# Optimization experiments

Measured on AMD Instinct MI355X. Metric: run time of the kernel, lower is better.

## Reference

```python
import jax, jax.numpy as jnp
import numpy as np

N = 100000      # nodes
E = 1600000     # edges (avg degree 16)
F_IN = 64       # num_features
HID = 16        # hidden channels (fixed in module)
OUT = 32        # num_classes
K = 2           # kernel_size (dim=1, degree=1 open B-spline -> 2 basis fns)


def setup_inputs() -> dict:
    key = jax.random.key(0)
    ks = jax.random.split(key, 8)
    return {
        "x": jax.random.normal(ks[0], (N, F_IN), jnp.float32),
        "edge_index": jax.random.randint(ks[1], (2, E), 0, N, dtype=jnp.int64),
        "dropout": 0,  # unused in eval mode (F.dropout training=False)
        "edge_attr": jnp.full((E, 1), 0.1, jnp.float32),  # nt([0.1]) broadcast per edge
        "W1": jax.random.normal(ks[2], (K, F_IN, HID), jnp.float32) / np.sqrt(K * F_IN).astype(np.float32),
        "root1": jax.random.normal(ks[3], (F_IN, HID), jnp.float32) / np.sqrt(F_IN).astype(np.float32),
        "bias1": jnp.zeros((HID,), jnp.float32),
        "W2": jax.random.normal(ks[4], (K, HID, OUT), jnp.float32) / np.sqrt(K * HID).astype(np.float32),
        "root2": jax.random.normal(ks[5], (HID, OUT), jnp.float32) / np.sqrt(HID).astype(np.float32),
        "bias2": jnp.zeros((OUT,), jnp.float32),
    }


def spline_conv(x, edge_index, edge_attr, W, root, bias):
    """SplineConv, dim=1, kernel_size=2, degree=1 open B-spline, aggr='mean'."""
    src, dst = edge_index[0], edge_index[1]
    n = x.shape[0]
    u = edge_attr[:, 0]                                  # [E] pseudo-coords in [0,1]
    # degree-1 open spline, kernel_size=2: frac = u*(ks-1) = u; kernels {0,1}
    basis = jnp.stack([1.0 - u, u], axis=1)              # [E, K]
    # transform at node level (cheaper than gathering raw features per edge)
    h = jnp.einsum('nf,kfo->nko', x, W)                  # [N, K, out]
    msg = jnp.einsum('ek,eko->eo', basis, h[src])        # [E, out]
    summed = jax.ops.segment_sum(msg, dst, num_segments=n)
    deg = jax.ops.segment_sum(jnp.ones_like(u), dst, num_segments=n)
    out = summed / jnp.maximum(deg, 1.0)[:, None]        # mean aggregation
    return out + x @ root + bias                          # root weight + bias


def reference(x, edge_index, dropout, edge_attr, W1, root1, bias1, W2, root2, bias2):
    # dropout is a no-op in eval mode
    h = jax.nn.elu(spline_conv(x, edge_index, edge_attr, W1, root1, bias1))
    h = spline_conv(h, edge_index, edge_attr, W2, root2, bias2)
    return jax.nn.log_softmax(h, axis=1)
```

## Files before the change

### kernel.cpp

```cpp
#include <hip/hip_runtime.h>
#include <math.h>

#define NN 100000
#define NE 1600000
#define F_IN 64
#define HID 16
#define OUTF 32
#define BKT_SHIFT 6
#define BKT_NODES 64
#define NBKT 1563
#define SRCM 0x1FFFF
#define CAP_REG 2048
#define CAP_LDS 1536
#define PBLK2 500
#define EPB2 3200
#define OVF_MAX 4096

__device__ __forceinline__ unsigned bf16r(float f) {
    unsigned u = __float_as_uint(f);
    return (u + 0x7FFFu + ((u >> 16) & 1u)) >> 16;
}
__device__ __forceinline__ float bfa(unsigned p) { return __uint_as_float(p << 16); }
__device__ __forceinline__ float bfd(unsigned p) { return __uint_as_float(p & 0xFFFF0000u); }
__device__ __forceinline__ float bfh(unsigned short v) { return __uint_as_float(((unsigned)v) << 16); }

__device__ __forceinline__ void acc8(uint4 hv, float u, float* s0, float* s1) {
    unsigned w[4] = {hv.x, hv.y, hv.z, hv.w};
#pragma unroll
    for (int q = 0; q < 4; ++q) {
        float lo = __uint_as_float(w[q] << 16);
        float hi = __uint_as_float(w[q] & 0xFFFF0000u);
        s0[2 * q]     += lo; s1[2 * q]     = fmaf(u, lo, s1[2 * q]);
        s0[2 * q + 1] += hi; s1[2 * q + 1] = fmaf(u, hi, s1[2 * q + 1]);
    }
}
__device__ __forceinline__ void acc4(uint4 ap, float u, float* a) {
    unsigned w[4] = {ap.x, ap.y, ap.z, ap.w};
#pragma unroll
    for (int q = 0; q < 4; ++q)
        a[q] += fmaf(u, bfd(w[q]), bfa(w[q]));
}

__global__ __launch_bounds__(256) void zeroG_kernel(int* __restrict__ gcur,
                                                    int* __restrict__ novf) {
    int t = blockIdx.x * 256 + threadIdx.x;
    if (t < NBKT) gcur[t] = 0;
    if (t == NBKT) novf[0] = 0;
}

__global__ __launch_bounds__(1024) void partF_kernel(const int* __restrict__ ei,
                                                     const float* __restrict__ ea,
                                                     int* __restrict__ gcur,
                                                     int* __restrict__ novf,
                                                     int4* __restrict__ ovf,
                                                     int2* __restrict__ bkt) {
    __shared__ int hcnt[NBKT];
    __shared__ int hbase[NBKT];
    __shared__ int lbase[NBKT];
    __shared__ int s[1024];
    __shared__ int2 sbuf[EPB2];
    __shared__ unsigned short bid[EPB2];
    int t = threadIdx.x, blk = blockIdx.x;
    for (int i = t; i < NBKT; i += 1024) hcnt[i] = 0;
    __syncthreads();
    int beg = blk * EPB2;
    int4 d4 = make_int4(0, 0, 0, 0);
    bool act = (4 * t) < EPB2;
    if (act) {
        d4 = *(const int4*)(ei + NE + beg + 4 * t);
        atomicAdd(&hcnt[d4.x >> BKT_SHIFT], 1);
        atomicAdd(&hcnt[d4.y >> BKT_SHIFT], 1);
        atomicAdd(&hcnt[d4.z >> BKT_SHIFT], 1);
        atomicAdd(&hcnt[d4.w >> BKT_SHIFT], 1);
    }
    __syncthreads();
    int i0 = 2 * t, i1 = 2 * t + 1;
    int v0 = (i0 < NBKT) ? hcnt[i0] : 0;
    int v1 = (i1 < NBKT) ? hcnt[i1] : 0;
    s[t] = v0 + v1;
    __syncthreads();
    for (int off = 1; off < 1024; off <<= 1) {
        int xv = (t >= off) ? s[t - off] : 0;
        __syncthreads();
        s[t] += xv;
        __syncthreads();
    }
    int run = (t == 0) ? 0 : s[t - 1];
    if (i0 < NBKT) lbase[i0] = run;
    if (i1 < NBKT) lbase[i1] = run + v0;
    __syncthreads();
    for (int i = t; i < NBKT; i += 1024) {
        int c = hcnt[i];
        hbase[i] = c ? atomicAdd(&gcur[i], c) : 0;
        hcnt[i] = 0;
    }
    __syncthreads();
    if (act) {
        int4 s4 = *(const int4*)(ei + beg + 4 * t);
        float4 u4 = *(const float4*)(ea + beg + 4 * t);
        int dst[4] = {d4.x, d4.y, d4.z, d4.w};
        int src[4] = {s4.x, s4.y, s4.z, s4.w};
        float uu[4] = {u4.x, u4.y, u4.z, u4.w};
#pragma unroll
        for (int k = 0; k < 4; ++k) {
            int b = dst[k] >> BKT_SHIFT;
            int r = atomicAdd(&hcnt[b], 1);
            int lp = lbase[b] + r;
            sbuf[lp] = make_int2(src[k] | ((dst[k] & (BKT_NODES - 1)) << 17),
                                 __float_as_int(uu[k]));
            bid[lp] = (unsigned short)b;
        }
    }
    __syncthreads();
    for (int i = t; i < EPB2; i += 1024) {
        int2 pk = sbuf[i];
        int b = bid[i];
        int p = hbase[b] + (i - lbase[b]);
        if (p < CAP_REG) {
            bkt[(size_t)b * CAP_REG + p] = pk;
        } else {
            int o = atomicAdd(novf, 1);
            if (o < OVF_MAX)
                ovf[o] = make_int4(b * BKT_NODES + (((unsigned)pk.x) >> 17), pk.x & SRCM, pk.y, 0);
        }
    }
}

__global__ __launch_bounds__(256) void proj1_kernel(const float* __restrict__ x,
                                                    const float* __restrict__ W1,
                                                    const float* __restrict__ root1,
                                                    const float* __restrict__ bias1,
                                                    unsigned* __restrict__ ab1p,
                                                    float* __restrict__ r1) {
    __shared__ float w[2 * F_IN * HID];
    __shared__ float wr[F_IN * HID];
    __shared__ float bb[HID];
    for (int i = threadIdx.x; i < 2 * F_IN * HID; i += 256) w[i] = W1[i];
    for (int i = threadIdx.x; i < F_IN * HID; i += 256) wr[i] = root1[i];
    if (threadIdx.x < HID) bb[threadIdx.x] = bias1[threadIdx.x];
    __syncthreads();
    int n = blockIdx.x * 256 + threadIdx.x;
    if (n >= NN) return;
    float accA[HID], accB[HID], accR[HID];
#pragma unroll
    for (int o = 0; o < HID; ++o) { accA[o] = 0.f; accB[o] = 0.f; accR[o] = bb[o]; }
    const float4* xr4 = (const float4*)(x + (size_t)n * F_IN);
    for (int f4 = 0; f4 < F_IN / 4; ++f4) {
        float4 xv4 = xr4[f4];
        float xs[4] = {xv4.x, xv4.y, xv4.z, xv4.w};
#pragma unroll
        for (int q = 0; q < 4; ++q) {
            int f = f4 * 4 + q;
            float xv = xs[q];
            const float* w0 = &w[f * HID];
            const float* w1 = &w[F_IN * HID + f * HID];
            const float* w2 = &wr[f * HID];
#pragma unroll
            for (int o = 0; o < HID; ++o) {
                accA[o] = fmaf(xv, w0[o], accA[o]);
                accB[o] = fmaf(xv, w1[o], accB[o]);
                accR[o] = fmaf(xv, w2[o], accR[o]);
            }
        }
    }
    unsigned* ar = ab1p + (size_t)n * HID;
    float* rr = r1 + (size_t)n * HID;
#pragma unroll
    for (int o = 0; o < HID; ++o) {
        ar[o] = bf16r(accA[o]) | (bf16r(accB[o] - accA[o]) << 16);
        rr[o] = accR[o];
    }
}

__global__ __launch_bounds__(256) void gather1_kernel(const int* __restrict__ gcur,
                                                      const int* __restrict__ novf,
                                                      const int4* __restrict__ ovf,
                                                      int2* __restrict__ bkt,
                                                      const unsigned* __restrict__ ab1p,
                                                      const float* __restrict__ r1,
                                                      unsigned short* __restrict__ h16,
                                                      float* __restrict__ dinv,
                                                      int* __restrict__ segg) {
    __shared__ int2 sorted[CAP_LDS];
    __shared__ int cnt[BKT_NODES], cur[BKT_NODES], segb[BKT_NODES + 1];
    __shared__ float degsL[BKT_NODES];
    int t = threadIdx.x;
    int b = blockIdx.x;
    int tot = gcur[b];
    int beg = b * CAP_REG;
    if (t < BKT_NODES) { cnt[t] = 0; cur[t] = 0; degsL[t] = 0.f; }
    __syncthreads();
    int nodeBase = b * BKT_NODES;

    if (tot <= CAP_LDS) {
        for (int e = t; e < tot; e += 256)
            atomicAdd(&cnt[((unsigned)bkt[beg + e].x) >> 17], 1);
        __syncthreads();
        if (t < BKT_NODES) {
            int v = cnt[t];
            int sc = v;
#pragma unroll
            for (int off = 1; off < 64; off <<= 1) {
                int o = __shfl_up(sc, off, 64);
                if (t >= off) sc += o;
            }
            segb[t] = sc - v;
            if (t == 63) segb[64] = sc;
        }
        __syncthreads();
        for (int e = t; e < tot; e += 256) {
            int2 pk = bkt[beg + e];
            int loc = ((unsigned)pk.x) >> 17;
            int pos = segb[loc] + atomicAdd(&cur[loc], 1);
            sorted[pos] = pk;
        }
        __syncthreads();
        int nv = tot >> 1;
        int4* s4 = (int4*)sorted;
        int4* o4 = (int4*)(bkt + beg);
        for (int i = t; i < nv; i += 256) o4[i] = s4[i];
        if (t == 0 && (tot & 1)) bkt[beg + tot - 1] = sorted[tot - 1];
        if (t <= BKT_NODES) segg[b * (BKT_NODES + 1) + t] = segb[t];
        int node = t >> 2;
        int jq = t & 3;
        int s0 = segb[node], e2 = segb[node + 1];
        float acc[4] = {0.f, 0.f, 0.f, 0.f};
        int e = s0;
        for (; e + 3 < e2; e += 4) {
            int2 p0 = sorted[e];
            int2 p1 = sorted[e + 1];
            int2 p2 = sorted[e + 2];
            int2 p3 = sorted[e + 3];
            uint4 a0 = *(const uint4*)(ab1p + ((size_t)(p0.x & SRCM) << 4) + (jq << 2));
            uint4 a1 = *(const uint4*)(ab1p + ((size_t)(p1.x & SRCM) << 4) + (jq << 2));
            uint4 a2 = *(const uint4*)(ab1p + ((size_t)(p2.x & SRCM) << 4) + (jq << 2));
            uint4 a3 = *(const uint4*)(ab1p + ((size_t)(p3.x & SRCM) << 4) + (jq << 2));
            acc4(a0, __int_as_float(p0.y), acc);
            acc4(a1, __int_as_float(p1.y), acc);
            acc4(a2, __int_as_float(p2.y), acc);
            acc4(a3, __int_as_float(p3.y), acc);
        }
        for (; e < e2; ++e) {
            int2 pk = sorted[e];
            uint4 ap = *(const uint4*)(ab1p + ((size_t)(pk.x & SRCM) << 4) + (jq << 2));
            acc4(ap, __int_as_float(pk.y), acc);
        }
        int n = nodeBase + node;
        if (n < NN) {
            float d0 = 1.f / (float)max(e2 - s0, 1);
            float4 rv = *(const float4*)(r1 + ((size_t)n << 4) + (jq << 2));
            float rr[4] = {rv.x, rv.y, rv.z, rv.w};
            unsigned hw[4];
#pragma unroll
            for (int k = 0; k < 4; ++k) {
                float v = acc[k] * d0 + rr[k];
                hw[k] = bf16r(v > 0.f ? v : expm1f(v));
            }
            *(uint2*)(h16 + ((size_t)n << 4) + (jq << 2)) =
                make_uint2(hw[0] | (hw[1] << 16), hw[2] | (hw[3] << 16));
            if (jq == 0) dinv[n] = d0;
        }
    } else {
        float* accL = (float*)sorted;
        int inreg = min(tot, CAP_REG);
        int end = beg + inreg;
        for (int i = t; i < BKT_NODES * HID; i += 256) accL[i] = 0.f;
        __syncthreads();
        int j = t & (HID - 1);
        int g = t >> 4;
        for (int e = beg + g; e < end; e += 16) {
            int2 pk = bkt[e];
            unsigned p = ab1p[(size_t)(pk.x & SRCM) * HID + j];
            atomicAdd(&accL[(((unsigned)pk.x) >> 17) * HID + j],
                      fmaf(__int_as_float(pk.y), bfd(p), bfa(p)));
            if (j == 0) atomicAdd(&degsL[((unsigned)pk.x) >> 17], 1.f);
        }
        int ovn = min(novf[0], OVF_MAX);
        for (int o = 0; o < ovn; ++o) {
            int4 ent = ovf[o];
            int loc = ent.x - nodeBase;
            if (loc >= 0 && loc < BKT_NODES && g == 0) {
                unsigned p = ab1p[(size_t)ent.y * HID + j];
                atomicAdd(&accL[loc * HID + j], fmaf(__int_as_float(ent.z), bfd(p), bfa(p)));
                if (j == 0) atomicAdd(&degsL[loc], 1.f);
            }
        }
        __syncthreads();
        if (t < BKT_NODES) degsL[t] = 1.f / fmaxf(degsL[t], 1.f);
        if (t == 0) segg[b * (BKT_NODES + 1)] = -1;
        __syncthreads();
        for (int idx = t; idx < BKT_NODES * HID; idx += 256) {
            int nl = idx >> 4, jj = idx & (HID - 1);
            int n = nodeBase + nl;
            if (n < NN) {
                float v = accL[idx] * degsL[nl] + r1[(size_t)n * HID + jj];
                h16[(size_t)n * HID + jj] = (unsigned short)bf16r(v > 0.f ? v : expm1f(v));
            }
        }
        if (t < BKT_NODES && nodeBase + t < NN) dinv[nodeBase + t] = degsL[t];
    }
}

#define HB_NODES 32
__global__ __launch_bounds__(256) void gather2_kernel(const int* __restrict__ gcur,
                                                      const int* __restrict__ novf,
                                                      const int4* __restrict__ ovf,
                                                      const int2* __restrict__ bkt,
                                                      const unsigned short* __restrict__ h16,
                                                      const float* __restrict__ W2,
                                                      const float* __restrict__ root2,
                                                      const float* __restrict__ bias2,
                                                      const float* __restrict__ dinv,
                                                      const int* __restrict__ segg,
                                                      float* __restrict__ out) {
    __shared__ int segb[HB_NODES + 1];
    __shared__ int sflag;
    __shared__ float s0L[HB_NODES * HID];
    __shared__ float s1L[HB_NODES * HID];
    __shared__ float hloc[HB_NODES * HID];
    __shared__ float w20[HID * OUTF], w2d[HID * OUTF], wr[HID * OUTF];
    __shared__ float bb[OUTF];
    int t = threadIdx.x;
    int b2 = blockIdx.x;
    int b = b2 >> 1;
    int h = b2 & 1;
    for (int i = t; i < HID * OUTF; i += 256) {
        float a = W2[i];
        w20[i] = a;
        w2d[i] = W2[HID * OUTF + i] - a;
        wr[i] = root2[i];
    }
    if (t < OUTF) bb[t] = bias2[t];
    int tot = gcur[b];
    int beg = b * CAP_REG;
    int nodeBase = b * BKT_NODES + h * HB_NODES;
    if (t <= HB_NODES) segb[t] = segg[b * (BKT_NODES + 1) + h * HB_NODES + t];
    if (t == 0) sflag = segg[b * (BKT_NODES + 1)];
    if (t < HB_NODES * HID / 8) {
        uint4 hv = *(const uint4*)(h16 + ((size_t)nodeBase << 4) + t * 8);
        unsigned w4[4] = {hv.x, hv.y, hv.z, hv.w};
#pragma unroll
        for (int q = 0; q < 4; ++q) {
            hloc[t * 8 + 2 * q]     = __uint_as_float(w4[q] << 16);
            hloc[t * 8 + 2 * q + 1] = __uint_as_float(w4[q] & 0xFFFF0000u);
        }
    }
    __syncthreads();

    if (tot <= CAP_LDS && sflag != -1) {
        const int2* sp = bkt + beg;
        int node = t >> 3;
        int sub = (t >> 1) & 3;
        int jh = t & 1;
        int s = segb[node], e2 = segb[node + 1];
        float s0[8] = {0.f, 0.f, 0.f, 0.f, 0.f, 0.f, 0.f, 0.f};
        float s1[8] = {0.f, 0.f, 0.f, 0.f, 0.f, 0.f, 0.f, 0.f};
        int e = s + sub;
        for (; e + 12 < e2; e += 16) {
            int2 p0 = sp[e];
            int2 p1 = sp[e + 4];
            int2 p2 = sp[e + 8];
            int2 p3 = sp[e + 12];
            uint4 h0 = *(const uint4*)(h16 + ((size_t)(p0.x & SRCM) << 4) + (jh << 3));
            uint4 h1 = *(const uint4*)(h16 + ((size_t)(p1.x & SRCM) << 4) + (jh << 3));
            uint4 h2 = *(const uint4*)(h16 + ((size_t)(p2.x & SRCM) << 4) + (jh << 3));
            uint4 h3 = *(const uint4*)(h16 + ((size_t)(p3.x & SRCM) << 4) + (jh << 3));
            acc8(h0, __int_as_float(p0.y), s0, s1);
            acc8(h1, __int_as_float(p1.y), s0, s1);
            acc8(h2, __int_as_float(p2.y), s0, s1);
            acc8(h3, __int_as_float(p3.y), s0, s1);
        }
        for (; e < e2; e += 4) {
            int2 pk = sp[e];
            uint4 hv = *(const uint4*)(h16 + ((size_t)(pk.x & SRCM) << 4) + (jh << 3));
            acc8(hv, __int_as_float(pk.y), s0, s1);
        }
#pragma unroll
        for (int k = 0; k < 8; ++k) {
            s0[k] += __shfl_xor(s0[k], 2); s0[k] += __shfl_xor(s0[k], 4);
            s1[k] += __shfl_xor(s1[k], 2); s1[k] += __shfl_xor(s1[k], 4);
        }
        if (sub == 0) {
            int base = node * HID + jh * 8;
#pragma unroll
            for (int k = 0; k < 8; ++k) { s0L[base + k] = s0[k]; s1L[base + k] = s1[k]; }
        }
        __syncthreads();
    } else {
        int inreg = min(tot, CAP_REG);
        int end = beg + inreg;
        for (int i = t; i < HB_NODES * HID; i += 256) { s0L[i] = 0.f; s1L[i] = 0.f; }
        __syncthreads();
        int j = t & (HID - 1);
        int g = t >> 4;
        for (int e = beg + g; e < end; e += 16) {
            int2 pk = bkt[e];
            int loc = ((unsigned)pk.x) >> 17;
            if ((loc >> 5) == h) {
                float hvv = bfh(h16[(size_t)(pk.x & SRCM) * HID + j]);
                atomicAdd(&s0L[(loc & 31) * HID + j], hvv);
                atomicAdd(&s1L[(loc & 31) * HID + j], __int_as_float(pk.y) * hvv);
            }
        }
        int ovn = min(novf[0], OVF_MAX);
        for (int o = 0; o < ovn; ++o) {
            int4 ent = ovf[o];
            int loc = ent.x - nodeBase;
            if (loc >= 0 && loc < HB_NODES && g == 0) {
                float hvv = bfh(h16[(size_t)ent.y * HID + j]);
                atomicAdd(&s0L[loc * HID + j], hvv);
                atomicAdd(&s1L[loc * HID + j], __int_as_float(ent.z) * hvv);
            }
        }
        __syncthreads();
    }

#pragma unroll
    for (int it = 0; it < HB_NODES * OUTF / 256; ++it) {
        int idx = it * 256 + t;
        int nl = idx >> 5, jj = idx & (OUTF - 1);
        int n = nodeBase + nl;
        float v = 0.f;
        if (n < NN) {
            float msum = 0.f;
            const float* S0 = &s0L[nl * HID];
            const float* S1 = &s1L[nl * HID];
#pragma unroll
            for (int f = 0; f < HID; ++f)
                msum += S0[f] * w20[f * OUTF + jj] + S1[f] * w2d[f * OUTF + jj];
            v = msum * dinv[n] + bb[jj];
            const float* hr = &hloc[nl * HID];
#pragma unroll
            for (int f = 0; f < HID; ++f)
                v = fmaf(hr[f], wr[f * OUTF + jj], v);
        }
        float m = v;
#pragma unroll
        for (int mask = 16; mask >= 1; mask >>= 1) m = fmaxf(m, __shfl_xor(m, mask));
        float ex = expf(v - m);
        float sm = ex;
#pragma unroll
        for (int mask = 16; mask >= 1; mask >>= 1) sm += __shfl_xor(sm, mask);
        if (n < NN) out[(size_t)n * OUTF + jj] = v - m - logf(sm);
    }
}

extern "C" void kernel_launch(void* const* d_in, const int* in_sizes, int n_in,
                              void* d_out, int out_size, void* d_ws, size_t ws_size,
                              hipStream_t stream) {
    const float* x     = (const float*)d_in[0];
    const int*   ei    = (const int*)d_in[1];
    const float* ea    = (const float*)d_in[3];
    const float* W1    = (const float*)d_in[4];
    const float* root1 = (const float*)d_in[5];
    const float* bias1 = (const float*)d_in[6];
    const float* W2    = (const float*)d_in[7];
    const float* root2 = (const float*)d_in[8];
    const float* bias2 = (const float*)d_in[9];
    float* out = (float*)d_out;
    float* ws  = (float*)d_ws;

    const size_t N = NN;
    int*            gcur = (int*)(ws);
    int*            novf = (int*)(ws + 2000);
    int4*           ovf  = (int4*)(ws + 2048);
    float*          dinv = ws + 20000;
    int*            segg = (int*)(ws + 120000);
    float*          r1   = ws + 222000;
    unsigned*       ab1p = (unsigned*)(ws + 222000 + 16 * N);
    unsigned short* h16  = (unsigned short*)(ws + 222000 + 32 * N);
    int2*           bkt  = (int2*)(ws + 222000 + 40 * N);

    int nbN = (NN + 255) / 256;
    zeroG_kernel<<<(NBKT + 256) / 256, 256, 0, stream>>>(gcur, novf);
    partF_kernel<<<PBLK2, 1024, 0, stream>>>(ei, ea, gcur, novf, ovf, bkt);
    proj1_kernel<<<nbN, 256, 0, stream>>>(x, W1, root1, bias1, ab1p, r1);
    gather1_kernel<<<NBKT, 256, 0, stream>>>(gcur, novf, ovf, bkt, ab1p, r1, h16, dinv, segg);
    gather2_kernel<<<NBKT * 2, 256, 0, stream>>>(gcur, novf, ovf, bkt, h16, W2, root2, bias2, dinv, segg, out);
}
```

Measured before the change: 120.0 us.

## Keep gathered sums in registers and compute epilogue per node-thread group

```diff
diff --git a/kernel.cpp b/kernel.cpp
--- a/kernel.cpp
+++ b/kernel.cpp
@@ -11,7 +11,7 @@
 #define NBKT 1563
 #define SRCM 0x1FFFF
 #define CAP_REG 2048
-#define CAP_LDS 1536
+#define CAP_LDS 1184
 #define PBLK2 500
 #define EPB2 3200
 #define OVF_MAX 4096
@@ -313,13 +313,10 @@
                                                       const float* __restrict__ dinv,
                                                       const int* __restrict__ segg,
                                                       float* __restrict__ out) {
+    __shared__ float w20[HID * OUTF], w2d[HID * OUTF], wr[HID * OUTF];
+    __shared__ float bb[OUTF];
     __shared__ int segb[HB_NODES + 1];
     __shared__ int sflag;
-    __shared__ float s0L[HB_NODES * HID];
-    __shared__ float s1L[HB_NODES * HID];
-    __shared__ float hloc[HB_NODES * HID];
-    __shared__ float w20[HID * OUTF], w2d[HID * OUTF], wr[HID * OUTF];
-    __shared__ float bb[OUTF];
     int t = threadIdx.x;
     int b2 = blockIdx.x;
     int b = b2 >> 1;
@@ -336,25 +333,18 @@
     int nodeBase = b * BKT_NODES + h * HB_NODES;
     if (t <= HB_NODES) segb[t] = segg[b * (BKT_NODES + 1) + h * HB_NODES + t];
     if (t == 0) sflag = segg[b * (BKT_NODES + 1)];
-    if (t < HB_NODES * HID / 8) {
-        uint4 hv = *(const uint4*)(h16 + ((size_t)nodeBase << 4) + t * 8);
-        unsigned w4[4] = {hv.x, hv.y, hv.z, hv.w};
-#pragma unroll
-        for (int q = 0; q < 4; ++q) {
-            hloc[t * 8 + 2 * q]     = __uint_as_float(w4[q] << 16);
-            hloc[t * 8 + 2 * q + 1] = __uint_as_float(w4[q] & 0xFFFF0000u);
-        }
-    }
-    __syncthreads();
+    __syncthreads();
+
+    int node = t >> 3;
+    int li = t & 7;
+    int sub = li >> 1;
+    int jh = li & 1;
+    float S0[8] = {0.f, 0.f, 0.f, 0.f, 0.f, 0.f, 0.f, 0.f};
+    float S1[8] = {0.f, 0.f, 0.f, 0.f, 0.f, 0.f, 0.f, 0.f};
 
     if (tot <= CAP_LDS && sflag != -1) {
         const int2* sp = bkt + beg;
-        int node = t >> 3;
-        int sub = (t >> 1) & 3;
-        int jh = t & 1;
         int s = segb[node], e2 = segb[node + 1];
-        float s0[8] = {0.f, 0.f, 0.f, 0.f, 0.f, 0.f, 0.f, 0.f};
-        float s1[8] = {0.f, 0.f, 0.f, 0.f, 0.f, 0.f, 0.f, 0.f};
         int e = s + sub;
         for (; e + 12 < e2; e += 16) {
             int2 p0 = sp[e];
@@ -365,34 +355,30 @@
             uint4 h1 = *(const uint4*)(h16 + ((size_t)(p1.x & SRCM) << 4) + (jh << 3));
             uint4 h2 = *(const uint4*)(h16 + ((size_t)(p2.x & SRCM) << 4) + (jh << 3));
             uint4 h3 = *(const uint4*)(h16 + ((size_t)(p3.x & SRCM) << 4) + (jh << 3));
-            acc8(h0, __int_as_float(p0.y), s0, s1);
-            acc8(h1, __int_as_float(p1.y), s0, s1);
-            acc8(h2, __int_as_float(p2.y), s0, s1);
-            acc8(h3, __int_as_float(p3.y), s0, s1);
+            acc8(h0, __int_as_float(p0.y), S0, S1);
+            acc8(h1, __int_as_float(p1.y), S0, S1);
+            acc8(h2, __int_as_float(p2.y), S0, S1);
+            acc8(h3, __int_as_float(p3.y), S0, S1);
         }
         for (; e < e2; e += 4) {
             int2 pk = sp[e];
             uint4 hv = *(const uint4*)(h16 + ((size_t)(pk.x & SRCM) << 4) + (jh << 3));
-            acc8(hv, __int_as_float(pk.y), s0, s1);
+            acc8(hv, __int_as_float(pk.y), S0, S1);
         }
 #pragma unroll
         for (int k = 0; k < 8; ++k) {
-            s0[k] += __shfl_xor(s0[k], 2); s0[k] += __shfl_xor(s0[k], 4);
-            s1[k] += __shfl_xor(s1[k], 2); s1[k] += __shfl_xor(s1[k], 4);
-        }
-        if (sub == 0) {
-            int base = node * HID + jh * 8;
-#pragma unroll
-            for (int k = 0; k < 8; ++k) { s0L[base + k] = s0[k]; s1L[base + k] = s1[k]; }
-        }
-        __syncthreads();
+            S0[k] += __shfl_xor(S0[k], 2); S0[k] += __shfl_xor(S0[k], 4);
+            S1[k] += __shfl_xor(S1[k], 2); S1[k] += __shfl_xor(S1[k], 4);
+        }
     } else {
+        float* s0L = w20;
+        float* s1L = w2d;
+        for (int i = t; i < HB_NODES * HID; i += 256) { s0L[i] = 0.f; s1L[i] = 0.f; }
+        __syncthreads();
+        int j = t & (HID - 1);
+        int g = t >> 4;
         int inreg = min(tot, CAP_REG);
         int end = beg + inreg;
-        for (int i = t; i < HB_NODES * HID; i += 256) { s0L[i] = 0.f; s1L[i] = 0.f; }
-        __syncthreads();
-        int j = t & (HID - 1);
-        int g = t >> 4;
         for (int e = beg + g; e < end; e += 16) {
             int2 pk = bkt[e];
             int loc = ((unsigned)pk.x) >> 17;
@@ -413,35 +399,70 @@
             }
         }
         __syncthreads();
-    }
-
-#pragma unroll
-    for (int it = 0; it < HB_NODES * OUTF / 256; ++it) {
-        int idx = it * 256 + t;
-        int nl = idx >> 5, jj = idx & (OUTF - 1);
-        int n = nodeBase + nl;
-        float v = 0.f;
-        if (n < NN) {
-            float msum = 0.f;
-            const float* S0 = &s0L[nl * HID];
-            const float* S1 = &s1L[nl * HID];
+#pragma unroll
+        for (int k = 0; k < 8; ++k) {
+            S0[k] = s0L[node * HID + jh * 8 + k];
+            S1[k] = s1L[node * HID + jh * 8 + k];
+        }
+        __syncthreads();
+        for (int i = t; i < HID * OUTF; i += 256) {
+            float a = W2[i];
+            w20[i] = a;
+            w2d[i] = W2[HID * OUTF + i] - a;
+        }
+        __syncthreads();
+    }
+
+    float F0[16], F1[16];
+#pragma unroll
+    for (int k = 0; k < 8; ++k) {
+        float p0 = __shfl_xor(S0[k], 1);
+        float p1 = __shfl_xor(S1[k], 1);
+        F0[k] = jh ? p0 : S0[k];
+        F0[8 + k] = jh ? S0[k] : p0;
+        F1[k] = jh ? p1 : S1[k];
+        F1[8 + k] = jh ? S1[k] : p1;
+    }
+    int n = nodeBase + node;
+    if (n < NN) {
+        float di = dinv[n];
+        uint4 hA = *(const uint4*)(h16 + ((size_t)n << 4));
+        uint4 hB = *(const uint4*)(h16 + ((size_t)n << 4) + 8);
+        float hf[16];
+        unsigned wa[4] = {hA.x, hA.y, hA.z, hA.w};
+        unsigned wb[4] = {hB.x, hB.y, hB.z, hB.w};
+#pragma unroll
+        for (int q = 0; q < 4; ++q) {
+            hf[2 * q]     = __uint_as_float(wa[q] << 16);
+            hf[2 * q + 1] = __uint_as_float(wa[q] & 0xFFFF0000u);
+            hf[8 + 2 * q]     = __uint_as_float(wb[q] << 16);
+            hf[8 + 2 * q + 1] = __uint_as_float(wb[q] & 0xFFFF0000u);
+        }
+        float outv[4];
+#pragma unroll
+        for (int q = 0; q < 4; ++q) {
+            int jj = li * 4 + q;
+            float ms = 0.f;
 #pragma unroll
             for (int f = 0; f < HID; ++f)
-                msum += S0[f] * w20[f * OUTF + jj] + S1[f] * w2d[f * OUTF + jj];
-            v = msum * dinv[n] + bb[jj];
-            const float* hr = &hloc[nl * HID];
+                ms += F0[f] * w20[f * OUTF + jj] + F1[f] * w2d[f * OUTF + jj];
+            float v = ms * di + bb[jj];
 #pragma unroll
             for (int f = 0; f < HID; ++f)
-                v = fmaf(hr[f], wr[f * OUTF + jj], v);
-        }
-        float m = v;
-#pragma unroll
-        for (int mask = 16; mask >= 1; mask >>= 1) m = fmaxf(m, __shfl_xor(m, mask));
-        float ex = expf(v - m);
-        float sm = ex;
-#pragma unroll
-        for (int mask = 16; mask >= 1; mask >>= 1) sm += __shfl_xor(sm, mask);
-        if (n < NN) out[(size_t)n * OUTF + jj] = v - m - logf(sm);
+                v = fmaf(hf[f], wr[f * OUTF + jj], v);
+            outv[q] = v;
+        }
+        float m = fmaxf(fmaxf(outv[0], outv[1]), fmaxf(outv[2], outv[3]));
+        m = fmaxf(m, __shfl_xor(m, 1));
+        m = fmaxf(m, __shfl_xor(m, 2));
+        m = fmaxf(m, __shfl_xor(m, 4));
+        float sl = expf(outv[0] - m) + expf(outv[1] - m) + expf(outv[2] - m) + expf(outv[3] - m);
+        sl += __shfl_xor(sl, 1);
+        sl += __shfl_xor(sl, 2);
+        sl += __shfl_xor(sl, 4);
+        float lse = m + logf(sl);
+        *(float4*)(out + (size_t)n * OUTF + li * 4) =
+            make_float4(outv[0] - lse, outv[1] - lse, outv[2] - lse, outv[3] - lse);
     }
 }
 
```

New measurement: 117.3 us. 1.02x faster.
